# Kernel optimization log

Hardware: AMD Instinct MI355X
Metric: run time of the kernel (lower is better)

Reference implementation:

```python
import jax, jax.numpy as jnp
import numpy as np

N = 100000
E = 1200000
D = 64
EPS = 1e-5  # BatchNorm1d default eps


def setup_inputs() -> dict:
    key = jax.random.key(0)
    ks = jax.random.split(key, 5)
    x = jax.random.normal(ks[0], (N, D), dtype=jnp.float32)
    edge_index = jax.random.randint(ks[1], (2, E), 0, N, dtype=jnp.int32)
    W1 = jax.random.normal(ks[2], (D, D), dtype=jnp.float32) * (1.0 / np.sqrt(D))
    W2 = jax.random.normal(ks[3], (D, D), dtype=jnp.float32) * (1.0 / np.sqrt(D))
    return {
        'x': x,
        'edge_index': edge_index,
        'W1': W1,
        'b1': jnp.zeros((D,), jnp.float32),
        'gamma1': jnp.ones((D,), jnp.float32),
        'beta1': jnp.zeros((D,), jnp.float32),
        'W2': W2,
        'b2': jnp.zeros((D,), jnp.float32),
        'gamma2': jnp.ones((D,), jnp.float32),
        'beta2': jnp.zeros((D,), jnp.float32),
    }


def gcn_conv(x, src, dst, W, b):
    # GCNConv: xw = x @ W; add self-loops; symmetric deg^{-1/2} normalization;
    # scatter-add aggregation over incoming edges; + bias.
    xw = x @ W  # [N, out]
    # degree including self-loop (edge weight 1)
    deg = jnp.zeros((x.shape[0],), x.dtype).at[dst].add(1.0) + 1.0  # [N]
    dinv = jax.lax.rsqrt(deg)
    norm = dinv[src] * dinv[dst]  # [E]
    agg = jnp.zeros_like(xw).at[dst].add(norm[:, None] * xw[src])
    agg = agg + (dinv * dinv)[:, None] * xw  # self-loop term: deg^{-1} * xw
    return agg + b


def batchnorm(x, gamma, beta):
    # training-mode BatchNorm1d over node dimension (biased variance)
    mu = x.mean(axis=0)
    var = x.var(axis=0)
    return gamma * (x - mu) * jax.lax.rsqrt(var + EPS) + beta


def reference(x, edge_index, W1, b1, gamma1, beta1, W2, b2, gamma2, beta2):
    src, dst = edge_index[0], edge_index[1]
    h = gcn_conv(x, src, dst, W1, b1)
    h = jax.nn.leaky_relu(batchnorm(h, gamma1, beta1), 0.01)
    # dropout p=0.0 -> identity
    h = gcn_conv(h, src, dst, W2, b2)
    h = jax.nn.leaky_relu(batchnorm(h, gamma2, beta2), 0.01)
    return h
```

## Files before the change

kernel.cpp:

```cpp
#include <hip/hip_runtime.h>
#include <hip/hip_bf16.h>

#define NN 100000
#define NE 1200000
#define DD 64
#define EPS 1e-5f

#define NB 196
#define GEMM_BLOCKS (NN / 32)
#define HIST_BLOCKS 256
#define PART_BLOCKS 256
#define EPH ((NE + HIST_BLOCKS - 1) / HIST_BLOCKS)
#define EPB ((NE + PART_BLOCKS - 1) / PART_BLOCKS)

template <bool BN>
__device__ __forceinline__ void gemm_tile(const float* __restrict__ X,
                                          const float* __restrict__ W,
                                          __hip_bfloat16* __restrict__ XWh,
                                          const float* __restrict__ stats,
                                          const float* __restrict__ gamma,
                                          const float* __restrict__ beta,
                                          int blk) {
    __shared__ float xs[32][64];
    __shared__ float sc_s[64], sh_s[64];
    int col = threadIdx.x & 63;
    int rg  = threadIdx.x >> 6;
    int row0 = blk * 32;

    if (BN) {
        if (threadIdx.x < 64) {
            const float inv_n = 1.0f / (float)NN;
            float mu  = stats[threadIdx.x] * inv_n;
            float var = stats[64 + threadIdx.x] * inv_n - mu * mu;
            float sc  = gamma[threadIdx.x] * rsqrtf(var + EPS);
            sc_s[threadIdx.x] = sc;
            sh_s[threadIdx.x] = beta[threadIdx.x] - sc * mu;
        }
        __syncthreads();
    }

    float w[64];
#pragma unroll
    for (int k = 0; k < 64; ++k) w[k] = W[k * 64 + col];

    for (int i = threadIdx.x; i < 32 * 16; i += 256) {
        int r = i >> 4, c4 = i & 15;
        float4 v = ((const float4*)(X + (size_t)(row0 + r) * 64))[c4];
        if (BN) {
            float4 s4 = ((const float4*)sc_s)[c4];
            float4 h4 = ((const float4*)sh_s)[c4];
            v.x = s4.x * v.x + h4.x; v.x = fmaxf(v.x, 0.01f * v.x);
            v.y = s4.y * v.y + h4.y; v.y = fmaxf(v.y, 0.01f * v.y);
            v.z = s4.z * v.z + h4.z; v.z = fmaxf(v.z, 0.01f * v.z);
            v.w = s4.w * v.w + h4.w; v.w = fmaxf(v.w, 0.01f * v.w);
        }
        ((float4*)&xs[r][0])[c4] = v;
    }
    __syncthreads();

    float acc[8];
#pragma unroll
    for (int r8 = 0; r8 < 8; ++r8) {
        int r = rg * 8 + r8;
        float a = 0.0f;
#pragma unroll
        for (int k = 0; k < 64; k += 4) {
            float4 xv = *((const float4*)&xs[r][k]);
            a += xv.x * w[k] + xv.y * w[k + 1] + xv.z * w[k + 2] + xv.w * w[k + 3];
        }
        acc[r8] = a;
    }
#pragma unroll
    for (int r8 = 0; r8 < 8; ++r8)
        XWh[(size_t)(row0 + rg * 8 + r8) * 64 + col] = __float2bfloat16(acc[r8]);
}

__global__ __launch_bounds__(256) void k_l1(const float* __restrict__ X,
                                            const float* __restrict__ W,
                                            __hip_bfloat16* __restrict__ XWh,
                                            const int* __restrict__ dst,
                                            int* __restrict__ cnt196) {
    if (blockIdx.x < HIST_BLOCKS) {
        __shared__ int h[NB];
        for (int t = threadIdx.x; t < NB; t += 256) h[t] = 0;
        __syncthreads();
        int s0 = blockIdx.x * EPH;
        int s1 = s0 + EPH; if (s1 > NE) s1 = NE;
        for (int i = s0 + threadIdx.x; i < s1; i += 256)
            atomicAdd(&h[dst[i] >> 9], 1);
        __syncthreads();
        for (int t = threadIdx.x; t < NB; t += 256)
            if (h[t]) atomicAdd(&cnt196[t], h[t]);
    } else {
        gemm_tile<false>(X, W, XWh, nullptr, nullptr, nullptr,
                         (int)blockIdx.x - HIST_BLOCKS);
    }
}

__global__ __launch_bounds__(256) void k_gemm2(const float* __restrict__ X,
                                               const float* __restrict__ W,
                                               __hip_bfloat16* __restrict__ XWh,
                                               const float* __restrict__ stats,
                                               const float* __restrict__ gamma,
                                               const float* __restrict__ beta) {
    gemm_tile<true>(X, W, XWh, stats, gamma, beta, blockIdx.x);
}

__global__ __launch_bounds__(256) void k_scanb(const int* __restrict__ cnt196,
                                               int* __restrict__ bo,
                                               int* __restrict__ cur) {
    __shared__ int s[256];
    int t = threadIdx.x;
    int v = (t < NB) ? cnt196[t] : 0;
    s[t] = v;
    __syncthreads();
    for (int o = 1; o < 256; o <<= 1) {
        int u = (t >= o) ? s[t - o] : 0;
        __syncthreads();
        s[t] += u;
        __syncthreads();
    }
    if (t < NB) {
        int ex = s[t] - v;
        bo[t] = ex;
        cur[t] = ex;
    }
    if (t == 0) bo[NB] = NE;
}

__global__ __launch_bounds__(256) void k_part(const int* __restrict__ src,
                                              const int* __restrict__ dst,
                                              int* __restrict__ cur,
                                              int* __restrict__ ebuf) {
    __shared__ int h[NB];
    for (int t = threadIdx.x; t < NB; t += 256) h[t] = 0;
    __syncthreads();
    int s0 = blockIdx.x * EPB;
    int s1 = s0 + EPB; if (s1 > NE) s1 = NE;
    for (int i = s0 + threadIdx.x; i < s1; i += 256)
        atomicAdd(&h[dst[i] >> 9], 1);
    __syncthreads();
    for (int t = threadIdx.x; t < NB; t += 256) {
        int c = h[t];
        h[t] = c ? atomicAdd(&cur[t], c) : 0;
    }
    __syncthreads();
    for (int i = s0 + threadIdx.x; i < s1; i += 256) {
        int d = dst[i];
        int p = atomicAdd(&h[d >> 9], 1);
        ebuf[p] = src[i] | ((d & 511) << 17);
    }
}

__global__ __launch_bounds__(512) void k_bucket(const int* __restrict__ ebuf,
                                                const int* __restrict__ bo,
                                                int* __restrict__ off,
                                                float* __restrict__ dinv,
                                                int* __restrict__ esrc) {
    __shared__ int s[512];
    int b = blockIdx.x, t = threadIdx.x;
    int base = b << 9;
    int e0 = bo[b], e1 = bo[b + 1];
    s[t] = 0;
    __syncthreads();
    for (int e = e0 + t; e < e1; e += 512)
        atomicAdd(&s[ebuf[e] >> 17], 1);
    __syncthreads();
    int deg = s[t];
    if (base + t < NN) dinv[base + t] = rsqrtf((float)deg + 1.0f);
    for (int o = 1; o < 512; o <<= 1) {
        int u = (t >= o) ? s[t - o] : 0;
        __syncthreads();
        s[t] += u;
        __syncthreads();
    }
    int gstart = e0 + s[t] - deg;
    if (base + t < NN) off[base + t] = gstart;
    if (b == NB - 1 && t == 0) off[NN] = NE;
    __syncthreads();
    s[t] = gstart;
    __syncthreads();
    for (int e = e0 + t; e < e1; e += 512) {
        int v = ebuf[e];
        int p = atomicAdd(&s[v >> 17], 1);
        esrc[p] = v & 0x1FFFF;
    }
}

__device__ __forceinline__ float4 bf16x4(uint2 u) {
    float4 f;
    f.x = __uint_as_float(u.x << 16);
    f.y = __uint_as_float(u.x & 0xFFFF0000u);
    f.z = __uint_as_float(u.y << 16);
    f.w = __uint_as_float(u.y & 0xFFFF0000u);
    return f;
}

__global__ __launch_bounds__(256) void k_agg(const __hip_bfloat16* __restrict__ XWh,
                                             const int* __restrict__ off,
                                             const int* __restrict__ esrc,
                                             const float* __restrict__ dinv,
                                             float* __restrict__ out) {
    const uint2* __restrict__ XW2 = (const uint2*)XWh;
    int node = blockIdx.x * 4 + (threadIdx.x >> 6);
    int lane = threadIdx.x & 63;
    int grp  = lane >> 4;
    int sub  = lane & 15;

    float di = dinv[node];
    float sl = (grp == 0) ? di : 0.0f;
    float4 self = bf16x4(XW2[(size_t)node * 16 + sub]);
    float4 a0 = make_float4(sl * self.x, sl * self.y, sl * self.z, sl * self.w);
    float4 a1 = make_float4(0.f, 0.f, 0.f, 0.f);
    float4 a2 = make_float4(0.f, 0.f, 0.f, 0.f);
    float4 a3 = make_float4(0.f, 0.f, 0.f, 0.f);

    int e0 = off[node], e1 = off[node + 1];
    int e = e0 + grp;
    for (; e + 12 < e1; e += 16) {
        int s0 = esrc[e];
        int s1 = esrc[e + 4];
        int s2 = esrc[e + 8];
        int s3 = esrc[e + 12];
        float n0 = dinv[s0], n1 = dinv[s1], n2 = dinv[s2], n3 = dinv[s3];
        float4 r0 = bf16x4(XW2[(size_t)s0 * 16 + sub]);
        float4 r1 = bf16x4(XW2[(size_t)s1 * 16 + sub]);
        float4 r2 = bf16x4(XW2[(size_t)s2 * 16 + sub]);
        float4 r3 = bf16x4(XW2[(size_t)s3 * 16 + sub]);
        a0.x += n0 * r0.x; a0.y += n0 * r0.y; a0.z += n0 * r0.z; a0.w += n0 * r0.w;
        a1.x += n1 * r1.x; a1.y += n1 * r1.y; a1.z += n1 * r1.z; a1.w += n1 * r1.w;
        a2.x += n2 * r2.x; a2.y += n2 * r2.y; a2.z += n2 * r2.z; a2.w += n2 * r2.w;
        a3.x += n3 * r3.x; a3.y += n3 * r3.y; a3.z += n3 * r3.z; a3.w += n3 * r3.w;
    }
    for (; e < e1; e += 4) {
        int s = esrc[e];
        float n = dinv[s];
        float4 r = bf16x4(XW2[(size_t)s * 16 + sub]);
        a0.x += n * r.x; a0.y += n * r.y; a0.z += n * r.z; a0.w += n * r.w;
    }
    a0.x += a1.x + a2.x + a3.x;
    a0.y += a1.y + a2.y + a3.y;
    a0.z += a1.z + a2.z + a3.z;
    a0.w += a1.w + a2.w + a3.w;

#pragma unroll
    for (int m = 16; m <= 32; m <<= 1) {
        a0.x += __shfl_xor(a0.x, m);
        a0.y += __shfl_xor(a0.y, m);
        a0.z += __shfl_xor(a0.z, m);
        a0.w += __shfl_xor(a0.w, m);
    }
    if (grp == 0) {
        a0.x *= di; a0.y *= di; a0.z *= di; a0.w *= di;
        ((float4*)out)[(size_t)node * 16 + sub] = a0;
    }
}

__global__ __launch_bounds__(256) void k_stats(const float* __restrict__ X,
                                               float* __restrict__ stats, int n) {
    __shared__ float ls[4][64], lq[4][64];
    int lane = threadIdx.x & 63, rg = threadIdx.x >> 6;
    float s = 0.0f, sq = 0.0f;
    for (int r = blockIdx.x * 4 + rg; r < n; r += gridDim.x * 4) {
        float v = X[(size_t)r * 64 + lane];
        s += v; sq += v * v;
    }
    ls[rg][lane] = s; lq[rg][lane] = sq;
    __syncthreads();
    if (rg == 0) {
        s  = ls[0][lane] + ls[1][lane] + ls[2][lane] + ls[3][lane];
        sq = lq[0][lane] + lq[1][lane] + lq[2][lane] + lq[3][lane];
        atomicAdd(&stats[lane], s);
        atomicAdd(&stats[64 + lane], sq);
    }
}

__global__ __launch_bounds__(256) void k_bnact(const float* __restrict__ X,
                                               float* __restrict__ Y,
                                               const float* __restrict__ stats,
                                               const float* __restrict__ gamma,
                                               const float* __restrict__ beta,
                                               int n) {
    int lane = threadIdx.x & 63, rg = threadIdx.x >> 6;
    float inv_n = 1.0f / (float)n;
    float mu  = stats[lane] * inv_n;
    float var = stats[64 + lane] * inv_n - mu * mu;
    float sc  = gamma[lane] * rsqrtf(var + EPS);
    float sh  = beta[lane] - sc * mu;
    for (int r = blockIdx.x * 4 + rg; r < n; r += gridDim.x * 4) {
        float v = X[(size_t)r * 64 + lane];
        v = sc * v + sh;
        Y[(size_t)r * 64 + lane] = fmaxf(v, 0.01f * v);
    }
}

extern "C" void kernel_launch(void* const* d_in, const int* in_sizes, int n_in,
                              void* d_out, int out_size, void* d_ws, size_t ws_size,
                              hipStream_t stream) {
    const float* x   = (const float*)d_in[0];
    const int*   ei  = (const int*)d_in[1];
    const int*   src = ei;
    const int*   dst = ei + NE;
    const float* W1  = (const float*)d_in[2];
    const float* g1  = (const float*)d_in[4];
    const float* be1 = (const float*)d_in[5];
    const float* W2  = (const float*)d_in[6];
    const float* g2  = (const float*)d_in[8];
    const float* be2 = (const float*)d_in[9];
    float* out = (float*)d_out;

    char* ws = (char*)d_ws;
    size_t p = 0;
    auto alloc = [&](size_t bytes) {
        size_t o = p;
        p = (p + bytes + 255) & ~(size_t)255;
        return o;
    };
    int*   zeroed  = (int*)(ws + alloc(2048));
    int*   cnt196  = zeroed;
    float* stats   = (float*)(zeroed + 256);
    int*   bo      = (int*)(ws + alloc((size_t)(NB + 1) * 4));
    int*   cur     = (int*)(ws + alloc((size_t)NB * 4));
    int*   ebuf    = (int*)(ws + alloc((size_t)NE * 4));
    int*   esrc    = (int*)(ws + alloc((size_t)NE * 4));
    int*   off     = (int*)(ws + alloc((size_t)(NN + 1) * 4));
    float* dinv    = (float*)(ws + alloc((size_t)NN * 4));
    __hip_bfloat16* Ah = (__hip_bfloat16*)(ws + alloc((size_t)NN * DD * 2));
    float* B       = (float*)(ws + alloc((size_t)NN * DD * 4));
    (void)ws_size; (void)in_sizes; (void)n_in; (void)out_size;

    hipMemsetAsync(zeroed, 0, 2048, stream);

    k_l1<<<HIST_BLOCKS + GEMM_BLOCKS, 256, 0, stream>>>(x, W1, Ah, dst, cnt196);
    k_scanb<<<1, 256, 0, stream>>>(cnt196, bo, cur);
    k_part<<<PART_BLOCKS, 256, 0, stream>>>(src, dst, cur, ebuf);
    k_bucket<<<NB, 512, 0, stream>>>(ebuf, bo, off, dinv, esrc);

    k_agg<<<NN / 4, 256, 0, stream>>>(Ah, off, esrc, dinv, B);
    k_stats<<<512, 256, 0, stream>>>(B, stats, NN);

    k_gemm2<<<GEMM_BLOCKS, 256, 0, stream>>>(B, W2, Ah, stats, g1, be1);
    k_agg<<<NN / 4, 256, 0, stream>>>(Ah, off, esrc, dinv, B);
    k_stats<<<512, 256, 0, stream>>>(B, stats + 128, NN);
    k_bnact<<<1024, 256, 0, stream>>>(B, out, stats + 128, g2, be2, NN);
}
```

Before: 319.8 us.

## Remap aggregation to 8-lane teams per node with 16-byte gathers

The aggregation kernel now gives each destination node 8 lanes, each loading 16 bytes (8 bf16 values) of the source row. The old kernel used a full 64-lane wave per node, split into 4 edge groups with a shuffle reduction at the end. The new mapping drops the cross-group shuffle and the idle lanes on low-degree nodes, and packs 32 nodes per block. The cost is less edge-level parallelism per node, so fewer gathers are in flight per lane and load is less balanced on high-degree nodes.

```diff
diff --git a/kernel.cpp b/kernel.cpp
--- a/kernel.cpp
+++ b/kernel.cpp
@@ -187,13 +187,15 @@
     }
 }
 
-__device__ __forceinline__ float4 bf16x4(uint2 u) {
-    float4 f;
-    f.x = __uint_as_float(u.x << 16);
-    f.y = __uint_as_float(u.x & 0xFFFF0000u);
-    f.z = __uint_as_float(u.y << 16);
-    f.w = __uint_as_float(u.y & 0xFFFF0000u);
-    return f;
+__device__ __forceinline__ void bf16x8(uint4 u, float* f) {
+    f[0] = __uint_as_float(u.x << 16);
+    f[1] = __uint_as_float(u.x & 0xFFFF0000u);
+    f[2] = __uint_as_float(u.y << 16);
+    f[3] = __uint_as_float(u.y & 0xFFFF0000u);
+    f[4] = __uint_as_float(u.z << 16);
+    f[5] = __uint_as_float(u.z & 0xFFFF0000u);
+    f[6] = __uint_as_float(u.w << 16);
+    f[7] = __uint_as_float(u.w & 0xFFFF0000u);
 }
 
 __global__ __launch_bounds__(256) void k_agg(const __hip_bfloat16* __restrict__ XWh,
@@ -201,59 +203,47 @@
                                              const int* __restrict__ esrc,
                                              const float* __restrict__ dinv,
                                              float* __restrict__ out) {
-    const uint2* __restrict__ XW2 = (const uint2*)XWh;
-    int node = blockIdx.x * 4 + (threadIdx.x >> 6);
-    int lane = threadIdx.x & 63;
-    int grp  = lane >> 4;
-    int sub  = lane & 15;
+    const uint4* __restrict__ XW4 = (const uint4*)XWh;
+    int team = threadIdx.x >> 3;
+    int sub  = threadIdx.x & 7;
+    int node = blockIdx.x * 32 + team;
 
     float di = dinv[node];
-    float sl = (grp == 0) ? di : 0.0f;
-    float4 self = bf16x4(XW2[(size_t)node * 16 + sub]);
-    float4 a0 = make_float4(sl * self.x, sl * self.y, sl * self.z, sl * self.w);
-    float4 a1 = make_float4(0.f, 0.f, 0.f, 0.f);
-    float4 a2 = make_float4(0.f, 0.f, 0.f, 0.f);
-    float4 a3 = make_float4(0.f, 0.f, 0.f, 0.f);
+    float a[8], b[8], r0[8], r1[8];
+    uint4 us = XW4[(size_t)node * 8 + sub];
+    bf16x8(us, a);
+#pragma unroll
+    for (int i = 0; i < 8; ++i) { a[i] *= di; b[i] = 0.0f; }
 
     int e0 = off[node], e1 = off[node + 1];
-    int e = e0 + grp;
-    for (; e + 12 < e1; e += 16) {
+    int e = e0;
+    for (; e + 1 < e1; e += 2) {
         int s0 = esrc[e];
-        int s1 = esrc[e + 4];
-        int s2 = esrc[e + 8];
-        int s3 = esrc[e + 12];
-        float n0 = dinv[s0], n1 = dinv[s1], n2 = dinv[s2], n3 = dinv[s3];
-        float4 r0 = bf16x4(XW2[(size_t)s0 * 16 + sub]);
-        float4 r1 = bf16x4(XW2[(size_t)s1 * 16 + sub]);
-        float4 r2 = bf16x4(XW2[(size_t)s2 * 16 + sub]);
-        float4 r3 = bf16x4(XW2[(size_t)s3 * 16 + sub]);
-        a0.x += n0 * r0.x; a0.y += n0 * r0.y; a0.z += n0 * r0.z; a0.w += n0 * r0.w;
-        a1.x += n1 * r1.x; a1.y += n1 * r1.y; a1.z += n1 * r1.z; a1.w += n1 * r1.w;
-        a2.x += n2 * r2.x; a2.y += n2 * r2.y; a2.z += n2 * r2.z; a2.w += n2 * r2.w;
-        a3.x += n3 * r3.x; a3.y += n3 * r3.y; a3.z += n3 * r3.z; a3.w += n3 * r3.w;
-    }
-    for (; e < e1; e += 4) {
-        int s = esrc[e];
-        float n = dinv[s];
-        float4 r = bf16x4(XW2[(size_t)s * 16 + sub]);
-        a0.x += n * r.x; a0.y += n * r.y; a0.z += n * r.z; a0.w += n * r.w;
-    }
-    a0.x += a1.x + a2.x + a3.x;
-    a0.y += a1.y + a2.y + a3.y;
-    a0.z += a1.z + a2.z + a3.z;
-    a0.w += a1.w + a2.w + a3.w;
-
-#pragma unroll
-    for (int m = 16; m <= 32; m <<= 1) {
-        a0.x += __shfl_xor(a0.x, m);
-        a0.y += __shfl_xor(a0.y, m);
-        a0.z += __shfl_xor(a0.z, m);
-        a0.w += __shfl_xor(a0.w, m);
-    }
-    if (grp == 0) {
-        a0.x *= di; a0.y *= di; a0.z *= di; a0.w *= di;
-        ((float4*)out)[(size_t)node * 16 + sub] = a0;
-    }
+        int s1 = esrc[e + 1];
+        float n0 = dinv[s0], n1 = dinv[s1];
+        uint4 u0 = XW4[(size_t)s0 * 8 + sub];
+        uint4 u1 = XW4[(size_t)s1 * 8 + sub];
+        bf16x8(u0, r0);
+        bf16x8(u1, r1);
+#pragma unroll
+        for (int i = 0; i < 8; ++i) a[i] += n0 * r0[i];
+#pragma unroll
+        for (int i = 0; i < 8; ++i) b[i] += n1 * r1[i];
+    }
+    if (e < e1) {
+        int s0 = esrc[e];
+        float n0 = dinv[s0];
+        uint4 u0 = XW4[(size_t)s0 * 8 + sub];
+        bf16x8(u0, r0);
+#pragma unroll
+        for (int i = 0; i < 8; ++i) a[i] += n0 * r0[i];
+    }
+#pragma unroll
+    for (int i = 0; i < 8; ++i) a[i] = (a[i] + b[i]) * di;
+
+    float4* o4 = (float4*)out;
+    o4[(size_t)node * 16 + sub * 2]     = make_float4(a[0], a[1], a[2], a[3]);
+    o4[(size_t)node * 16 + sub * 2 + 1] = make_float4(a[4], a[5], a[6], a[7]);
 }
 
 __global__ __launch_bounds__(256) void k_stats(const float* __restrict__ X,
@@ -336,11 +326,11 @@
     k_part<<<PART_BLOCKS, 256, 0, stream>>>(src, dst, cur, ebuf);
     k_bucket<<<NB, 512, 0, stream>>>(ebuf, bo, off, dinv, esrc);
 
-    k_agg<<<NN / 4, 256, 0, stream>>>(Ah, off, esrc, dinv, B);
+    k_agg<<<NN / 32, 256, 0, stream>>>(Ah, off, esrc, dinv, B);
     k_stats<<<512, 256, 0, stream>>>(B, stats, NN);
 
     k_gemm2<<<GEMM_BLOCKS, 256, 0, stream>>>(B, W2, Ah, stats, g1, be1);
-    k_agg<<<NN / 4, 256, 0, stream>>>(Ah, off, esrc, dinv, B);
+    k_agg<<<NN / 32, 256, 0, stream>>>(Ah, off, esrc, dinv, B);
     k_stats<<<512, 256, 0, stream>>>(B, stats + 128, NN);
     k_bnact<<<1024, 256, 0, stream>>>(B, out, stats + 128, g2, be2, NN);
 }
```

Result: faster. 288.4 us (-9.8%).
